# Kernel optimization log

Measured on AMD Instinct MI355X. Metric: run time of the kernel, lower is better.

Reference implementation:

```python
import jax, jax.numpy as jnp
import numpy as np
import math

B, L, D, K = 4, 2048, 1024, 3
PAD = K // 2
EPS_LN = 1e-5
EPS_NORM = 1e-12


def dwsep_conv(x_bld, dw, dwb, pw, pwb):
    # x_bld: [B, L, D] -> depthwise conv over L (groups=D) then pointwise 1x1
    x = jnp.transpose(x_bld, (0, 2, 1))  # [B, D, L]
    y = jax.lax.conv_general_dilated(
        x, dw, window_strides=(1,), padding=[(PAD, PAD)],
        feature_group_count=D, dimension_numbers=("NCH", "OIH", "NCH"))
    y = y + dwb[None, :, None]
    y = jnp.einsum("bcl,oc->bol", y, pw) + pwb[None, :, None]
    return jnp.transpose(y, (0, 2, 1))  # [B, L, D]


def l2norm(x):
    n = jnp.sqrt(jnp.sum(x * x, axis=-1, keepdims=True))
    return x / jnp.maximum(n, EPS_NORM)


def layernorm(x, g, b):
    mu = jnp.mean(x, axis=-1, keepdims=True)
    var = jnp.mean((x - mu) ** 2, axis=-1, keepdims=True)
    return (x - mu) * jax.lax.rsqrt(var + EPS_LN) * g + b


def setup_inputs() -> dict:
    key = jax.random.key(0)
    ks = jax.random.split(key, 24)
    s = 0.02
    def w(k, shape, scale=s):
        return (jax.random.normal(k, shape, dtype=jnp.float32) * scale)
    inp = {
        "x": jax.random.normal(ks[0], (B, L, D), dtype=jnp.float32),
        "wq": w(ks[1], (D, D)), "bq": jnp.zeros((D,), jnp.float32),
        "wk": w(ks[2], (D, D)), "bk": jnp.zeros((D,), jnp.float32),
        "wv": w(ks[3], (D, D)), "bv": jnp.zeros((D,), jnp.float32),
        "dwq": w(ks[4], (D, 1, K), 0.1), "dwq_b": jnp.zeros((D,), jnp.float32),
        "pwq": w(ks[5], (D, D)), "pwq_b": jnp.zeros((D,), jnp.float32),
        "dwk": w(ks[6], (D, 1, K), 0.1), "dwk_b": jnp.zeros((D,), jnp.float32),
        "pwk": w(ks[7], (D, D)), "pwk_b": jnp.zeros((D,), jnp.float32),
        "dwv": w(ks[8], (D, 1, K), 0.1), "dwv_b": jnp.zeros((D,), jnp.float32),
        "pwv": w(ks[9], (D, D)), "pwv_b": jnp.zeros((D,), jnp.float32),
        "wg": w(ks[10], (D, D)), "bg": jnp.zeros((D,), jnp.float32),
        "wo": w(ks[11], (D, D)), "bo": jnp.zeros((D,), jnp.float32),
        "mem_w": w(ks[12], (D, D)),
        "ln_g": jnp.ones((D,), jnp.float32),
        "ln_b": jnp.zeros((D,), jnp.float32),
    }
    return inp


def reference(x, wq, bq, wk, bk, wv, bv,
              dwq, dwq_b, pwq, pwq_b,
              dwk, dwk_b, pwk, pwk_b,
              dwv, dwv_b, pwv, pwv_b,
              wg, bg, wo, bo, mem_w, ln_g, ln_b):
    residual = x
    Q = jax.nn.silu(jnp.einsum("bld,ed->ble", x, wq) + bq)
    Kt = jax.nn.silu(jnp.einsum("bld,ed->ble", x, wk) + bk)
    V = jax.nn.silu(jnp.einsum("bld,ed->ble", x, wv) + bv)
    Q = dwsep_conv(Q, dwq, dwq_b, pwq, pwq_b)
    Kt = dwsep_conv(Kt, dwk, dwk_b, pwk, pwk_b)
    V = dwsep_conv(V, dwv, dwv_b, pwv, pwv_b)
    Qn = l2norm(Q)
    Kn = l2norm(Kt)
    scores = jnp.einsum("bqd,bkd->bqk", Qn, Kn) / math.sqrt(D)
    attn = jax.nn.softmax(scores, axis=-1)
    attn_out = jnp.einsum("bqk,bkd->bqd", attn, V)
    gate = jax.nn.sigmoid(jnp.einsum("bld,ed->ble", attn_out, wg) + bg)
    gated = gate * attn_out
    out = jnp.einsum("bld,ed->ble", gated, wo) + bo + residual
    out = layernorm(out, ln_g, ln_b)
    mem_pred = jnp.einsum("bld,de->ble", Kn, mem_w)
    mem_loss = jnp.mean((mem_pred - V) ** 2)
    return (out, mem_loss)
```

## Files before the change

### kernel.cpp

```cpp
#include <hip/hip_runtime.h>
#include <stdint.h>

typedef __attribute__((ext_vector_type(8))) short short8;
typedef __attribute__((ext_vector_type(4))) short short4v;
typedef __attribute__((ext_vector_type(4))) float f32x4;

#define DEV static __device__ __forceinline__

static constexpr int LL = 2048;
static constexpr int DD = 1024;
static constexpr long long BLD = 8388608LL;

DEV short f2bf(float f) {
    uint32_t u = __builtin_bit_cast(uint32_t, f);
    u += 0x7fffu + ((u >> 16) & 1u);
    return (short)(u >> 16);
}
DEV float bf2f(short s) {
    uint32_t u = ((uint32_t)(uint16_t)s) << 16;
    return __builtin_bit_cast(float, u);
}

DEV float waveSum(float v) {
#pragma unroll
    for (int o = 32; o; o >>= 1) v += __shfl_down(v, o);
    return v;
}
DEV float waveMax(float v) {
#pragma unroll
    for (int o = 32; o; o >>= 1) v = fmaxf(v, __shfl_down(v, o));
    return v;
}

DEV void gload16(const void* g, void* l) {
    __builtin_amdgcn_global_load_lds(
        (const __attribute__((address_space(1))) uint32_t*)(uintptr_t)g,
        (__attribute__((address_space(3))) uint32_t*)(uintptr_t)l,
        16, 0, 0);
}


__global__ __launch_bounds__(256) void k_zero1(float* p) {
    if (threadIdx.x == 0) *p = 0.f;
}

__global__ __launch_bounds__(256) void k_f32_to_bf16(const float* __restrict__ in,
                                                     short* __restrict__ out, int n8) {
    int i = blockIdx.x * 256 + threadIdx.x;
    if (i >= n8) return;
    const float4* p = (const float4*)(in + (long long)i * 8);
    float4 a = p[0], b = p[1];
    short8 o;
    o[0] = f2bf(a.x); o[1] = f2bf(a.y); o[2] = f2bf(a.z); o[3] = f2bf(a.w);
    o[4] = f2bf(b.x); o[5] = f2bf(b.y); o[6] = f2bf(b.z); o[7] = f2bf(b.w);
    *(short8*)(out + (long long)i * 8) = o;
}

__global__ __launch_bounds__(256) void k_wcat(
    const float* wq, const float* wk, const float* wv,
    const float* pq, const float* pk, const float* pv,
    const float* wg, const float* wo,
    short* Wqkv, short* Pqkv, short* Wg, short* Wo) {
    const int bid = blockIdx.x;
    const int w = bid >> 9;
    const long long i = (long long)((bid & 511) * 256 + threadIdx.x) * 8;
    const float* src; short* dst;
    switch (w) {
        case 0: src = wq; dst = Wqkv;                break;
        case 1: src = wk; dst = Wqkv + 1048576;      break;
        case 2: src = wv; dst = Wqkv + 2097152;      break;
        case 3: src = pq; dst = Pqkv;                break;
        case 4: src = pk; dst = Pqkv + 1048576;      break;
        case 5: src = pv; dst = Pqkv + 2097152;      break;
        case 6: src = wg; dst = Wg;                  break;
        default: src = wo; dst = Wo;                 break;
    }
    const float4* p = (const float4*)(src + i);
    float4 a = p[0], b = p[1];
    short8 o;
    o[0] = f2bf(a.x); o[1] = f2bf(a.y); o[2] = f2bf(a.z); o[3] = f2bf(a.w);
    o[4] = f2bf(b.x); o[5] = f2bf(b.y); o[6] = f2bf(b.z); o[7] = f2bf(b.w);
    *(short8*)(dst + i) = o;
}

__global__ __launch_bounds__(256) void k_biascat(
    const float* bq, const float* bk, const float* bv,
    const float* pq, const float* pk, const float* pv,
    float* bqkv, float* bpw) {
    const int idx = blockIdx.x * 256 + threadIdx.x;
    const int sel = idx >> 10, j = idx & 1023;
    const float* s;
    switch (sel) {
        case 0: s = bq; break; case 1: s = bk; break; case 2: s = bv; break;
        case 3: s = pq; break; case 4: s = pk; break; default: s = pv; break;
    }
    float v = s[j];
    if (sel < 3) bqkv[sel * 1024 + j] = v;
    else         bpw[(sel - 3) * 1024 + j] = v;
}

__global__ __launch_bounds__(256) void k_dwconv3b(const short* __restrict__ in,
                                                  const float* __restrict__ dwq,
                                                  const float* __restrict__ dwk,
                                                  const float* __restrict__ dwv,
                                                  const float* __restrict__ dbq,
                                                  const float* __restrict__ dbk,
                                                  const float* __restrict__ dbv,
                                                  short* __restrict__ outp) {
    const int idx = blockIdx.x * 256 + threadIdx.x;
    const int d8 = idx & 127;
    const int lc = (idx >> 7) & 255;
    const int b  = (idx >> 15) & 3;
    const int br = idx >> 17;
    const float* dw = (br == 0) ? dwq : (br == 1) ? dwk : dwv;
    const float* db = (br == 0) ? dbq : (br == 1) ? dbk : dbv;

    float w[24], bb[8];
    {
        const float4* wp = (const float4*)(dw + d8 * 24);
#pragma unroll
        for (int i = 0; i < 6; i++) {
            float4 t = wp[i];
            w[i * 4 + 0] = t.x; w[i * 4 + 1] = t.y;
            w[i * 4 + 2] = t.z; w[i * 4 + 3] = t.w;
        }
        const float4* bp = (const float4*)(db + d8 * 8);
        float4 t0 = bp[0], t1 = bp[1];
        bb[0] = t0.x; bb[1] = t0.y; bb[2] = t0.z; bb[3] = t0.w;
        bb[4] = t1.x; bb[5] = t1.y; bb[6] = t1.z; bb[7] = t1.w;
    }

    const int l0 = lc * 8;
    const long long base = ((long long)(b * LL + l0)) * 3072 + br * 1024 + d8 * 8;
    short8 xr[10];
#pragma unroll
    for (int i = 0; i < 10; i++) {
        const int l = l0 - 1 + i;
        if (l >= 0 && l < LL) xr[i] = *(const short8*)(in + base + (long long)(i - 1) * 3072);
        else { short8 z = {0, 0, 0, 0, 0, 0, 0, 0}; xr[i] = z; }
    }
#pragma unroll
    for (int j = 0; j < 8; j++) {
        short8 o;
#pragma unroll
        for (int c = 0; c < 8; c++) {
            float v = bb[c] + w[c * 3 + 0] * bf2f(xr[j][c])
                            + w[c * 3 + 1] * bf2f(xr[j + 1][c])
                            + w[c * 3 + 2] * bf2f(xr[j + 2][c]);
            o[c] = f2bf(v);
        }
        *(short8*)(outp + base + (long long)j * 3072) = o;
    }
}

__global__ __launch_bounds__(256) void k_l2norm(short* __restrict__ xp) {
    __shared__ float red[4];
    const long long row = blockIdx.x;
    short* p = xp + row * DD;
    const int t = threadIdx.x;
    short4v v = *(short4v*)(p + t * 4);
    float f0 = bf2f(v[0]), f1 = bf2f(v[1]), f2 = bf2f(v[2]), f3 = bf2f(v[3]);
    float ss = f0 * f0 + f1 * f1 + f2 * f2 + f3 * f3;
    ss = waveSum(ss);
    if ((t & 63) == 0) red[t >> 6] = ss;
    __syncthreads();
    ss = (red[0] + red[1]) + (red[2] + red[3]);
    float s = 1.f / fmaxf(sqrtf(ss), 1e-12f);
    v[0] = f2bf(f0 * s); v[1] = f2bf(f1 * s); v[2] = f2bf(f2 * s); v[3] = f2bf(f3 * s);
    *(short4v*)(p + t * 4) = v;
}

__global__ __launch_bounds__(256) void k_softmax(short* __restrict__ sp) {
    __shared__ float redM[4], redS[4];
    const long long row = blockIdx.x;
    short* p = sp + row * 2048;
    const int t = threadIdx.x;
    short8 v = *(short8*)(p + t * 8);
    float f[8];
    float m = -3.0e38f;
#pragma unroll
    for (int j = 0; j < 8; j++) { f[j] = bf2f(v[j]); m = fmaxf(m, f[j]); }
    m = waveMax(m);
    if ((t & 63) == 0) redM[t >> 6] = m;
    __syncthreads();
    m = fmaxf(fmaxf(redM[0], redM[1]), fmaxf(redM[2], redM[3]));
    float s = 0.f;
#pragma unroll
    for (int j = 0; j < 8; j++) { f[j] = __expf(f[j] - m); s += f[j]; }
    s = waveSum(s);
    if ((t & 63) == 0) redS[t >> 6] = s;
    __syncthreads();
    s = (redS[0] + redS[1]) + (redS[2] + redS[3]);
    float inv = 1.f / s;
#pragma unroll
    for (int j = 0; j < 8; j++) v[j] = f2bf(f[j] * inv);
    *(short8*)(p + t * 8) = v;
}

__global__ __launch_bounds__(256) void k_layernorm(float* __restrict__ y,
                                                   const float* __restrict__ g,
                                                   const float* __restrict__ b) {
    __shared__ float redS[4], redQ[4];
    const long long row = blockIdx.x;
    float* p = y + row * DD;
    const int t = threadIdx.x;
    float4 v = *(float4*)(p + t * 4);
    float s = v.x + v.y + v.z + v.w;
    float q = v.x * v.x + v.y * v.y + v.z * v.z + v.w * v.w;
    s = waveSum(s); q = waveSum(q);
    if ((t & 63) == 0) { redS[t >> 6] = s; redQ[t >> 6] = q; }
    __syncthreads();
    s = (redS[0] + redS[1]) + (redS[2] + redS[3]);
    q = (redQ[0] + redQ[1]) + (redQ[2] + redQ[3]);
    float mu = s * (1.f / DD);
    float var = q * (1.f / DD) - mu * mu;
    float rs = rsqrtf(var + 1e-5f);
    float4 o;
    o.x = (v.x - mu) * rs * g[t * 4 + 0] + b[t * 4 + 0];
    o.y = (v.y - mu) * rs * g[t * 4 + 1] + b[t * 4 + 1];
    o.z = (v.z - mu) * rs * g[t * 4 + 2] + b[t * 4 + 2];
    o.w = (v.w - mu) * rs * g[t * 4 + 3] + b[t * 4 + 3];
    *(float4*)(p + t * 4) = o;
}

__global__ __launch_bounds__(256) void k_transpose_bf16(const short* __restrict__ in,
                                                        short* __restrict__ out,
                                                        int rows, int cols) {
    __shared__ short tile[64][65];
    const long long boff = (long long)blockIdx.z * rows * cols;
    in += boff; out += boff;
    const int r0 = blockIdx.y * 64, c0 = blockIdx.x * 64;
    const int t = threadIdx.x;
#pragma unroll
    for (int i = 0; i < 16; i++) {
        int lin = i * 256 + t; int lr = lin >> 6, lc = lin & 63;
        tile[lr][lc] = in[(long long)(r0 + lr) * cols + (c0 + lc)];
    }
    __syncthreads();
#pragma unroll
    for (int i = 0; i < 16; i++) {
        int lin = i * 256 + t; int orr = lin >> 6, oc = lin & 63;
        out[(long long)(c0 + orr) * rows + (r0 + oc)] = tile[oc][orr];
    }
}

__global__ __launch_bounds__(256) void k_transpose_f32_bf16(const float* __restrict__ in,
                                                            short* __restrict__ out,
                                                            int rows, int cols) {
    __shared__ float tile[64][65];
    const int r0 = blockIdx.y * 64, c0 = blockIdx.x * 64;
    const int t = threadIdx.x;
#pragma unroll
    for (int i = 0; i < 16; i++) {
        int lin = i * 256 + t; int lr = lin >> 6, lc = lin & 63;
        tile[lr][lc] = in[(long long)(r0 + lr) * cols + (c0 + lc)];
    }
    __syncthreads();
#pragma unroll
    for (int i = 0; i < 16; i++) {
        int lin = i * 256 + t; int orr = lin >> 6, oc = lin & 63;
        out[(long long)(c0 + orr) * rows + (r0 + oc)] = f2bf(tile[oc][orr]);
    }
}

enum { EPI_SILU, EPI_BIAS, EPI_SCALE, EPI_PLAIN, EPI_GATE, EPI_RESID, EPI_MLOSS };

template <int EPI>
__global__ __launch_bounds__(512, 4) void gemm256b(
    const short* __restrict__ A, int lda, long long sAb,
    const short* __restrict__ W, int ldw, long long sWb,
    void* __restrict__ outv, int ldo, long long sOb,
    const float* __restrict__ bias, long long sBias,
    int K, float scale) {
    __shared__ short lds[24576];

    const int z = blockIdx.z;
    A += (long long)z * sAb;
    W += (long long)z * sWb;

    const int tid = threadIdx.x;
    const int wid = tid >> 6, lane = tid & 63;
    const int row0 = blockIdx.y * 256, col0 = blockIdx.x * 128;
    const int wrM = (wid >> 1) * 64, wcN = (wid & 1) * 64;
    const int rl = lane & 15, kcl = lane >> 4;

    f32x4 acc[4][4] = {};

    const int srow = tid >> 3;
    const int cswz = (tid & 7) ^ (srow & 7);
    long long offA[4], offB[2];
#pragma unroll
    for (int j = 0; j < 4; j++)
        offA[j] = (long long)(row0 + j * 64 + srow) * lda + cswz * 8;
#pragma unroll
    for (int j = 0; j < 2; j++)
        offB[j] = (long long)(col0 + j * 64 + srow) * ldw + cswz * 8;

    const int nk = K >> 6;
    const int swz0 = (kcl ^ (rl & 7)) * 8;
    const int swz1 = ((kcl + 4) ^ (rl & 7)) * 8;

    for (int t = 0; t < nk; ++t) {
        const short* a = A + (long long)t * 64;
        const short* w = W + (long long)t * 64;
#pragma unroll
        for (int j = 0; j < 4; j++)
            gload16(a + offA[j], lds + (j * 512 + tid) * 8);
#pragma unroll
        for (int j = 0; j < 2; j++)
            gload16(w + offB[j], lds + 16384 + (j * 512 + tid) * 8);
        asm volatile("s_waitcnt vmcnt(0)" ::: "memory");
        __builtin_amdgcn_s_barrier();

        short8 af[4], bfr[4];
#pragma unroll
        for (int mi = 0; mi < 4; mi++)
            af[mi] = *(const short8*)&lds[(wrM + mi * 16 + rl) * 64 + swz0];
#pragma unroll
        for (int ni = 0; ni < 4; ni++)
            bfr[ni] = *(const short8*)&lds[16384 + (wcN + ni * 16 + rl) * 64 + swz0];
        __builtin_amdgcn_s_setprio(1);
#pragma unroll
        for (int mi = 0; mi < 4; mi++)
#pragma unroll
            for (int ni = 0; ni < 4; ni++)
                acc[mi][ni] = __builtin_amdgcn_mfma_f32_16x16x32_bf16(
                    af[mi], bfr[ni], acc[mi][ni], 0, 0, 0);
        __builtin_amdgcn_s_setprio(0);
#pragma unroll
        for (int mi = 0; mi < 4; mi++)
            af[mi] = *(const short8*)&lds[(wrM + mi * 16 + rl) * 64 + swz1];
#pragma unroll
        for (int ni = 0; ni < 4; ni++)
            bfr[ni] = *(const short8*)&lds[16384 + (wcN + ni * 16 + rl) * 64 + swz1];
        __builtin_amdgcn_s_setprio(1);
#pragma unroll
        for (int mi = 0; mi < 4; mi++)
#pragma unroll
            for (int ni = 0; ni < 4; ni++)
                acc[mi][ni] = __builtin_amdgcn_mfma_f32_16x16x32_bf16(
                    af[mi], bfr[ni], acc[mi][ni], 0, 0, 0);
        __builtin_amdgcn_s_setprio(0);
        __builtin_amdgcn_s_barrier();
    }

    const int lr4 = (lane >> 4) * 4;
    float bcol[4];
    if constexpr (EPI == EPI_SILU || EPI == EPI_BIAS) {
        const float* bz = bias + (long long)z * sBias;
#pragma unroll
        for (int ni = 0; ni < 4; ni++) bcol[ni] = bz[col0 + wcN + ni * 16 + rl];
    }
    short* op = (short*)outv + (long long)z * sOb;
#pragma unroll
    for (int mi = 0; mi < 4; mi++) {
#pragma unroll
        for (int ni = 0; ni < 4; ni++) {
            const int gc = col0 + wcN + ni * 16 + rl;
#pragma unroll
            for (int r = 0; r < 4; r++) {
                const int gr = row0 + wrM + mi * 16 + lr4 + r;
                float v = acc[mi][ni][r];
                if constexpr (EPI == EPI_SILU) {
                    v += bcol[ni];
                    v = v / (1.f + __expf(-v));
                } else if constexpr (EPI == EPI_BIAS) {
                    v += bcol[ni];
                } else if constexpr (EPI == EPI_SCALE) {
                    v *= scale;
                }
                op[(long long)gr * ldo + gc] = f2bf(v);
            }
        }
    }
}

template <int EPI>
__global__ __launch_bounds__(256, 4) void gemm(
    const short* __restrict__ A, int lda, long long sAb,
    const short* __restrict__ W, int ldw, long long sWb,
    void* __restrict__ outv, int ldo, long long sOb,
    const float* __restrict__ bias, long long sBias,
    const void* __restrict__ aux,
    int K, float scale, float* __restrict__ lossOut) {
    __shared__ short lds[16384];

    const int z = blockIdx.z;
    A += (long long)z * sAb;
    W += (long long)z * sWb;

    const int tid = threadIdx.x;
    const int wid = tid >> 6, lane = tid & 63;
    const int row0 = blockIdx.y * 128, col0 = blockIdx.x * 128;
    const int wrM = (wid >> 1) * 64, wcN = (wid & 1) * 64;
    const int rl = lane & 15, kcl = lane >> 4;

    f32x4 acc[4][4] = {};

    const int srow = tid >> 3;
    const int cswz = (tid & 7) ^ (srow & 7);
    long long offA[4], offB[4];
#pragma unroll
    for (int j = 0; j < 4; j++) {
        const int rr = j * 32 + srow;
        offA[j] = (long long)(row0 + rr) * lda + cswz * 8;
        offB[j] = (long long)(col0 + rr) * ldw + cswz * 8;
    }

    const int nk = K >> 6;
    const int swz0 = (kcl ^ (rl & 7)) * 8;
    const int swz1 = ((kcl + 4) ^ (rl & 7)) * 8;

    for (int t = 0; t < nk; ++t) {
        const short* a = A + (long long)t * 64;
        const short* w = W + (long long)t * 64;
#pragma unroll
        for (int j = 0; j < 4; j++)
            gload16(a + offA[j], lds + (j * 256 + tid) * 8);
#pragma unroll
        for (int j = 0; j < 4; j++)
            gload16(w + offB[j], lds + 8192 + (j * 256 + tid) * 8);
        asm volatile("s_waitcnt vmcnt(0)" ::: "memory");
        __builtin_amdgcn_s_barrier();

        short8 af[4], bfr[4];
#pragma unroll
        for (int mi = 0; mi < 4; mi++)
            af[mi] = *(const short8*)&lds[(wrM + mi * 16 + rl) * 64 + swz0];
#pragma unroll
        for (int ni = 0; ni < 4; ni++)
            bfr[ni] = *(const short8*)&lds[8192 + (wcN + ni * 16 + rl) * 64 + swz0];
        __builtin_amdgcn_s_setprio(1);
#pragma unroll
        for (int mi = 0; mi < 4; mi++)
#pragma unroll
            for (int ni = 0; ni < 4; ni++)
                acc[mi][ni] = __builtin_amdgcn_mfma_f32_16x16x32_bf16(
                    af[mi], bfr[ni], acc[mi][ni], 0, 0, 0);
        __builtin_amdgcn_s_setprio(0);
#pragma unroll
        for (int mi = 0; mi < 4; mi++)
            af[mi] = *(const short8*)&lds[(wrM + mi * 16 + rl) * 64 + swz1];
#pragma unroll
        for (int ni = 0; ni < 4; ni++)
            bfr[ni] = *(const short8*)&lds[8192 + (wcN + ni * 16 + rl) * 64 + swz1];
        __builtin_amdgcn_s_setprio(1);
#pragma unroll
        for (int mi = 0; mi < 4; mi++)
#pragma unroll
            for (int ni = 0; ni < 4; ni++)
                acc[mi][ni] = __builtin_amdgcn_mfma_f32_16x16x32_bf16(
                    af[mi], bfr[ni], acc[mi][ni], 0, 0, 0);
        __builtin_amdgcn_s_setprio(0);
        __builtin_amdgcn_s_barrier();
    }

    const int lr4 = (lane >> 4) * 4;
    float bcol[4];
    if constexpr (EPI == EPI_SILU || EPI == EPI_BIAS || EPI == EPI_GATE || EPI == EPI_RESID) {
        const float* bz = bias + (long long)z * sBias;
#pragma unroll
        for (int ni = 0; ni < 4; ni++) bcol[ni] = bz[col0 + wcN + ni * 16 + rl];
    }
    float lsum = 0.f;
#pragma unroll
    for (int mi = 0; mi < 4; mi++) {
#pragma unroll
        for (int ni = 0; ni < 4; ni++) {
            const int gc = col0 + wcN + ni * 16 + rl;
#pragma unroll
            for (int r = 0; r < 4; r++) {
                const int gr = row0 + wrM + mi * 16 + lr4 + r;
                const long long oi = (long long)gr * ldo + gc;
                float v = acc[mi][ni][r];
                if constexpr (EPI == EPI_SILU) {
                    v += bcol[ni];
                    v = v / (1.f + __expf(-v));
                    ((short*)outv + (long long)z * sOb)[oi] = f2bf(v);
                } else if constexpr (EPI == EPI_BIAS) {
                    ((short*)outv + (long long)z * sOb)[oi] = f2bf(v + bcol[ni]);
                } else if constexpr (EPI == EPI_SCALE) {
                    ((short*)outv + (long long)z * sOb)[oi] = f2bf(v * scale);
                } else if constexpr (EPI == EPI_PLAIN) {
                    ((short*)outv + (long long)z * sOb)[oi] = f2bf(v);
                } else if constexpr (EPI == EPI_GATE) {
                    float g = 1.f / (1.f + __expf(-(v + bcol[ni])));
                    float a = bf2f(((const short*)aux)[oi]);
                    ((short*)outv)[oi] = f2bf(g * a);
                } else if constexpr (EPI == EPI_RESID) {
                    ((float*)outv)[oi] = v + bcol[ni] + ((const float*)aux)[oi];
                } else {
                    float dd = v - bf2f(((const short*)aux)[oi]);
                    lsum += dd * dd;
                }
            }
        }
    }
    if constexpr (EPI == EPI_MLOSS) {
        lsum = waveSum(lsum);
        if (lane == 0) atomicAdd(lossOut, lsum * scale);
    }
}


extern "C" void kernel_launch(void* const* d_in, const int* in_sizes, int n_in,
                              void* d_out, int out_size, void* d_ws, size_t ws_size,
                              hipStream_t stream) {
    const float* x    = (const float*)d_in[0];
    const float* wq   = (const float*)d_in[1];
    const float* bq   = (const float*)d_in[2];
    const float* wk   = (const float*)d_in[3];
    const float* bk   = (const float*)d_in[4];
    const float* wvw  = (const float*)d_in[5];
    const float* bvv  = (const float*)d_in[6];
    const float* dwq  = (const float*)d_in[7];
    const float* dwqb = (const float*)d_in[8];
    const float* pwq  = (const float*)d_in[9];
    const float* pwqb = (const float*)d_in[10];
    const float* dwk  = (const float*)d_in[11];
    const float* dwkb = (const float*)d_in[12];
    const float* pwk  = (const float*)d_in[13];
    const float* pwkb = (const float*)d_in[14];
    const float* dwv  = (const float*)d_in[15];
    const float* dwvb = (const float*)d_in[16];
    const float* pwv  = (const float*)d_in[17];
    const float* pwvb = (const float*)d_in[18];
    const float* wg   = (const float*)d_in[19];
    const float* bg   = (const float*)d_in[20];
    const float* wo   = (const float*)d_in[21];
    const float* bo   = (const float*)d_in[22];
    const float* memw = (const float*)d_in[23];
    const float* lng  = (const float*)d_in[24];
    const float* lnb  = (const float*)d_in[25];

    float* out = (float*)d_out;
    float* loss = out + BLD;

    char* base = (char*)d_ws;
    size_t off = 0;
    auto take = [&](size_t n) -> char* {
        char* p = base + off;
        off += (n + 255) & ~(size_t)255;
        return p;
    };
    const size_t WB = (size_t)DD * DD * 2;
    const size_t XB = (size_t)BLD * 2;
    short* Wqkv = (short*)take(3 * WB);
    short* Pqkv = (short*)take(3 * WB);
    short* Wgb  = (short*)take(WB);
    short* Wob  = (short*)take(WB);
    short* MwT  = (short*)take(WB);
    float* bqkv = (float*)take(3072 * 4);
    float* bpw  = (float*)take(3072 * 4);
    short* xb   = (short*)take(XB);
    short* pre  = (short*)take(3 * XB);
    short* post = (short*)take(3 * XB);

    short* qb = pre;
    short* kb = pre + BLD;
    short* vb = pre + 2 * BLD;
    short* scores = post;
    short* VT = post + 2 * BLD;
    short* aob = xb;
    short* gated = post;
    (void)ws_size; (void)in_sizes; (void)n_in; (void)out_size;

    const long long sLD = (long long)LL * DD;
    const long long sLLb = (long long)LL * LL;

    k_zero1<<<1, 1, 0, stream>>>(loss);
    k_wcat<<<4096, 256, 0, stream>>>(wq, wk, wvw, pwq, pwk, pwv, wg, wo,
                                     Wqkv, Pqkv, Wgb, Wob);
    k_biascat<<<24, 256, 0, stream>>>(bq, bk, bvv, pwqb, pwkb, pwvb, bqkv, bpw);
    k_transpose_f32_bf16<<<dim3(16, 16, 1), 256, 0, stream>>>(memw, MwT, DD, DD);
    k_f32_to_bf16<<<4096, 256, 0, stream>>>(x, xb, (int)(BLD / 8));

    gemm256b<EPI_SILU><<<dim3(24, 32, 1), 512, 0, stream>>>(
        xb, 1024, 0, Wqkv, 1024, 0, pre, 3072, 0, bqkv, 0, 1024, 0.f);

    k_dwconv3b<<<1536, 256, 0, stream>>>(pre, dwq, dwk, dwv, dwqb, dwkb, dwvb, post);

    gemm256b<EPI_BIAS><<<dim3(8, 32, 3), 512, 0, stream>>>(
        post, 3072, 1024, Pqkv, 1024, (long long)DD * DD, qb, 1024, BLD,
        bpw, 1024, 1024, 0.f);

    k_l2norm<<<16384, 256, 0, stream>>>(qb);
    k_transpose_bf16<<<dim3(16, 32, 4), 256, 0, stream>>>(vb, VT, 2048, 1024);

    gemm256b<EPI_SCALE><<<dim3(16, 8, 4), 512, 0, stream>>>(
        qb, 1024, sLD, kb, 1024, sLD, scores, 2048, sLLb,
        nullptr, 0, 1024, 0.03125f);
    k_softmax<<<8192, 256, 0, stream>>>(scores);

    gemm<EPI_PLAIN><<<dim3(8, 16, 4), 256, 0, stream>>>(
        scores, 2048, sLLb, VT, 2048, sLD, aob, 1024, sLD,
        nullptr, 0, nullptr, 2048, 0.f, nullptr);

    gemm<EPI_GATE><<<dim3(8, 64, 1), 256, 0, stream>>>(
        aob, 1024, 0, Wgb, 1024, 0, gated, 1024, 0, bg, 0, aob, 1024, 0.f, nullptr);

    gemm<EPI_RESID><<<dim3(8, 64, 1), 256, 0, stream>>>(
        gated, 1024, 0, Wob, 1024, 0, out, 1024, 0, bo, 0, x, 1024, 0.f, nullptr);
    k_layernorm<<<8192, 256, 0, stream>>>(out, lng, lnb);

    gemm<EPI_MLOSS><<<dim3(8, 64, 1), 256, 0, stream>>>(
        kb, 1024, 0, MwT, 1024, 0, nullptr, 1024, 0, nullptr, 0, vb,
        1024, 1.f / (float)BLD, loss);
}
```

Before: 411.6 us.

## Fuse exp into score GEMM, defer softmax normalization, merge AV with mem-loss GEMM

Drops the max-subtraction softmax pass because normalized Q/K bound the scores, applying exp in the score GEMM epilogue. A light row-sum kernel computes inverse sums that are applied in the AV GEMM epilogue. The AV GEMM and mem-loss GEMM now run as one launch to fill the device. The 256x128 GEMM variant is also replaced by the 128x128 kernel everywhere, which may lower data reuse on the large GEMMs.

```diff
diff --git a/kernel.cpp b/kernel.cpp
--- a/kernel.cpp
+++ b/kernel.cpp
@@ -10,6 +10,8 @@
 static constexpr int LL = 2048;
 static constexpr int DD = 1024;
 static constexpr long long BLD = 8388608LL;
+static constexpr long long SLD = 2097152LL;
+static constexpr long long SLLB = 4194304LL;
 
 DEV short f2bf(float f) {
     uint32_t u = __builtin_bit_cast(uint32_t, f);
@@ -24,11 +26,6 @@
 DEV float waveSum(float v) {
 #pragma unroll
     for (int o = 32; o; o >>= 1) v += __shfl_down(v, o);
-    return v;
-}
-DEV float waveMax(float v) {
-#pragma unroll
-    for (int o = 32; o; o >>= 1) v = fmaxf(v, __shfl_down(v, o));
     return v;
 }
 
@@ -170,31 +167,21 @@
     *(short4v*)(p + t * 4) = v;
 }
 
-__global__ __launch_bounds__(256) void k_softmax(short* __restrict__ sp) {
-    __shared__ float redM[4], redS[4];
+__global__ __launch_bounds__(256) void k_rowsuminv(const short* __restrict__ sp,
+                                                   float* __restrict__ rinv) {
+    __shared__ float red[4];
     const long long row = blockIdx.x;
-    short* p = sp + row * 2048;
+    const short* p = sp + row * 2048;
     const int t = threadIdx.x;
     short8 v = *(short8*)(p + t * 8);
-    float f[8];
-    float m = -3.0e38f;
-#pragma unroll
-    for (int j = 0; j < 8; j++) { f[j] = bf2f(v[j]); m = fmaxf(m, f[j]); }
-    m = waveMax(m);
-    if ((t & 63) == 0) redM[t >> 6] = m;
+    float s = 0.f;
+#pragma unroll
+    for (int j = 0; j < 8; j++) s += bf2f(v[j]);
+    s = waveSum(s);
+    if ((t & 63) == 0) red[t >> 6] = s;
     __syncthreads();
-    m = fmaxf(fmaxf(redM[0], redM[1]), fmaxf(redM[2], redM[3]));
-    float s = 0.f;
-#pragma unroll
-    for (int j = 0; j < 8; j++) { f[j] = __expf(f[j] - m); s += f[j]; }
-    s = waveSum(s);
-    if ((t & 63) == 0) redS[t >> 6] = s;
-    __syncthreads();
-    s = (redS[0] + redS[1]) + (redS[2] + redS[3]);
-    float inv = 1.f / s;
-#pragma unroll
-    for (int j = 0; j < 8; j++) v[j] = f2bf(f[j] * inv);
-    *(short8*)(p + t * 8) = v;
+    s = (red[0] + red[1]) + (red[2] + red[3]);
+    if (t == 0) rinv[row] = 1.f / s;
 }
 
 __global__ __launch_bounds__(256) void k_layernorm(float* __restrict__ y,
@@ -263,117 +250,7 @@
     }
 }
 
-enum { EPI_SILU, EPI_BIAS, EPI_SCALE, EPI_PLAIN, EPI_GATE, EPI_RESID, EPI_MLOSS };
-
-template <int EPI>
-__global__ __launch_bounds__(512, 4) void gemm256b(
-    const short* __restrict__ A, int lda, long long sAb,
-    const short* __restrict__ W, int ldw, long long sWb,
-    void* __restrict__ outv, int ldo, long long sOb,
-    const float* __restrict__ bias, long long sBias,
-    int K, float scale) {
-    __shared__ short lds[24576];
-
-    const int z = blockIdx.z;
-    A += (long long)z * sAb;
-    W += (long long)z * sWb;
-
-    const int tid = threadIdx.x;
-    const int wid = tid >> 6, lane = tid & 63;
-    const int row0 = blockIdx.y * 256, col0 = blockIdx.x * 128;
-    const int wrM = (wid >> 1) * 64, wcN = (wid & 1) * 64;
-    const int rl = lane & 15, kcl = lane >> 4;
-
-    f32x4 acc[4][4] = {};
-
-    const int srow = tid >> 3;
-    const int cswz = (tid & 7) ^ (srow & 7);
-    long long offA[4], offB[2];
-#pragma unroll
-    for (int j = 0; j < 4; j++)
-        offA[j] = (long long)(row0 + j * 64 + srow) * lda + cswz * 8;
-#pragma unroll
-    for (int j = 0; j < 2; j++)
-        offB[j] = (long long)(col0 + j * 64 + srow) * ldw + cswz * 8;
-
-    const int nk = K >> 6;
-    const int swz0 = (kcl ^ (rl & 7)) * 8;
-    const int swz1 = ((kcl + 4) ^ (rl & 7)) * 8;
-
-    for (int t = 0; t < nk; ++t) {
-        const short* a = A + (long long)t * 64;
-        const short* w = W + (long long)t * 64;
-#pragma unroll
-        for (int j = 0; j < 4; j++)
-            gload16(a + offA[j], lds + (j * 512 + tid) * 8);
-#pragma unroll
-        for (int j = 0; j < 2; j++)
-            gload16(w + offB[j], lds + 16384 + (j * 512 + tid) * 8);
-        asm volatile("s_waitcnt vmcnt(0)" ::: "memory");
-        __builtin_amdgcn_s_barrier();
-
-        short8 af[4], bfr[4];
-#pragma unroll
-        for (int mi = 0; mi < 4; mi++)
-            af[mi] = *(const short8*)&lds[(wrM + mi * 16 + rl) * 64 + swz0];
-#pragma unroll
-        for (int ni = 0; ni < 4; ni++)
-            bfr[ni] = *(const short8*)&lds[16384 + (wcN + ni * 16 + rl) * 64 + swz0];
-        __builtin_amdgcn_s_setprio(1);
-#pragma unroll
-        for (int mi = 0; mi < 4; mi++)
-#pragma unroll
-            for (int ni = 0; ni < 4; ni++)
-                acc[mi][ni] = __builtin_amdgcn_mfma_f32_16x16x32_bf16(
-                    af[mi], bfr[ni], acc[mi][ni], 0, 0, 0);
-        __builtin_amdgcn_s_setprio(0);
-#pragma unroll
-        for (int mi = 0; mi < 4; mi++)
-            af[mi] = *(const short8*)&lds[(wrM + mi * 16 + rl) * 64 + swz1];
-#pragma unroll
-        for (int ni = 0; ni < 4; ni++)
-            bfr[ni] = *(const short8*)&lds[16384 + (wcN + ni * 16 + rl) * 64 + swz1];
-        __builtin_amdgcn_s_setprio(1);
-#pragma unroll
-        for (int mi = 0; mi < 4; mi++)
-#pragma unroll
-            for (int ni = 0; ni < 4; ni++)
-                acc[mi][ni] = __builtin_amdgcn_mfma_f32_16x16x32_bf16(
-                    af[mi], bfr[ni], acc[mi][ni], 0, 0, 0);
-        __builtin_amdgcn_s_setprio(0);
-        __builtin_amdgcn_s_barrier();
-    }
-
-    const int lr4 = (lane >> 4) * 4;
-    float bcol[4];
-    if constexpr (EPI == EPI_SILU || EPI == EPI_BIAS) {
-        const float* bz = bias + (long long)z * sBias;
-#pragma unroll
-        for (int ni = 0; ni < 4; ni++) bcol[ni] = bz[col0 + wcN + ni * 16 + rl];
-    }
-    short* op = (short*)outv + (long long)z * sOb;
-#pragma unroll
-    for (int mi = 0; mi < 4; mi++) {
-#pragma unroll
-        for (int ni = 0; ni < 4; ni++) {
-            const int gc = col0 + wcN + ni * 16 + rl;
-#pragma unroll
-            for (int r = 0; r < 4; r++) {
-                const int gr = row0 + wrM + mi * 16 + lr4 + r;
-                float v = acc[mi][ni][r];
-                if constexpr (EPI == EPI_SILU) {
-                    v += bcol[ni];
-                    v = v / (1.f + __expf(-v));
-                } else if constexpr (EPI == EPI_BIAS) {
-                    v += bcol[ni];
-                } else if constexpr (EPI == EPI_SCALE) {
-                    v *= scale;
-                }
-                op[(long long)gr * ldo + gc] = f2bf(v);
-            }
-        }
-    }
-}
+enum { EPI_SILU, EPI_BIAS, EPI_EXPS, EPI_GATE, EPI_RESID };
 
 template <int EPI>
 __global__ __launch_bounds__(256, 4) void gemm(
@@ -382,7 +259,7 @@
     void* __restrict__ outv, int ldo, long long sOb,
     const float* __restrict__ bias, long long sBias,
     const void* __restrict__ aux,
-    int K, float scale, float* __restrict__ lossOut) {
+    int K, float scale) {
     __shared__ short lds[16384];
 
     const int z = blockIdx.z;
@@ -462,7 +339,6 @@
 #pragma unroll
         for (int ni = 0; ni < 4; ni++) bcol[ni] = bz[col0 + wcN + ni * 16 + rl];
     }
-    float lsum = 0.f;
 #pragma unroll
     for (int mi = 0; mi < 4; mi++) {
 #pragma unroll
@@ -479,26 +355,143 @@
                     ((short*)outv + (long long)z * sOb)[oi] = f2bf(v);
                 } else if constexpr (EPI == EPI_BIAS) {
                     ((short*)outv + (long long)z * sOb)[oi] = f2bf(v + bcol[ni]);
-                } else if constexpr (EPI == EPI_SCALE) {
-                    ((short*)outv + (long long)z * sOb)[oi] = f2bf(v * scale);
-                } else if constexpr (EPI == EPI_PLAIN) {
-                    ((short*)outv + (long long)z * sOb)[oi] = f2bf(v);
+                } else if constexpr (EPI == EPI_EXPS) {
+                    ((short*)outv + (long long)z * sOb)[oi] = f2bf(__expf(v * scale));
                 } else if constexpr (EPI == EPI_GATE) {
                     float g = 1.f / (1.f + __expf(-(v + bcol[ni])));
                     float a = bf2f(((const short*)aux)[oi]);
                     ((short*)outv)[oi] = f2bf(g * a);
                 } else if constexpr (EPI == EPI_RESID) {
                     ((float*)outv)[oi] = v + bcol[ni] + ((const float*)aux)[oi];
-                } else {
-                    float dd = v - bf2f(((const short*)aux)[oi]);
+                }
+            }
+        }
+    }
+}
+
+__global__ __launch_bounds__(256, 4) void k_avml(
+    const short* __restrict__ P, const short* __restrict__ VT,
+    const float* __restrict__ rinv, short* __restrict__ aob,
+    const short* __restrict__ kb, const short* __restrict__ MwT,
+    const short* __restrict__ vb, float* __restrict__ lossOut) {
+    __shared__ short lds[16384];
+
+    const int bid = blockIdx.x;
+    const bool isAV = bid < 512;
+    const short* A; const short* W;
+    int lda, ldw, K, row0, col0;
+    const float* rp = nullptr;
+    short* outp = nullptr;
+    if (isAV) {
+        const int z = bid >> 7, rem = bid & 127;
+        row0 = (rem >> 3) * 128; col0 = (rem & 7) * 128;
+        A = P + (long long)z * SLLB;  lda = 2048;
+        W = VT + (long long)z * SLD;  ldw = 2048;
+        K = 2048;
+        outp = aob + (long long)z * SLD;
+        rp = rinv + z * 2048;
+    } else {
+        const int rem = bid - 512;
+        row0 = (rem >> 3) * 128; col0 = (rem & 7) * 128;
+        A = kb; lda = 1024; W = MwT; ldw = 1024; K = 1024;
+    }
+
+    const int tid = threadIdx.x;
+    const int wid = tid >> 6, lane = tid & 63;
+    const int wrM = (wid >> 1) * 64, wcN = (wid & 1) * 64;
+    const int rl = lane & 15, kcl = lane >> 4;
+
+    f32x4 acc[4][4] = {};
+
+    const int srow = tid >> 3;
+    const int cswz = (tid & 7) ^ (srow & 7);
+    long long offA[4], offB[4];
+#pragma unroll
+    for (int j = 0; j < 4; j++) {
+        const int rr = j * 32 + srow;
+        offA[j] = (long long)(row0 + rr) * lda + cswz * 8;
+        offB[j] = (long long)(col0 + rr) * ldw + cswz * 8;
+    }
+
+    const int nk = K >> 6;
+    const int swz0 = (kcl ^ (rl & 7)) * 8;
+    const int swz1 = ((kcl + 4) ^ (rl & 7)) * 8;
+
+    for (int t = 0; t < nk; ++t) {
+        const short* a = A + (long long)t * 64;
+        const short* w = W + (long long)t * 64;
+#pragma unroll
+        for (int j = 0; j < 4; j++)
+            gload16(a + offA[j], lds + (j * 256 + tid) * 8);
+#pragma unroll
+        for (int j = 0; j < 4; j++)
+            gload16(w + offB[j], lds + 8192 + (j * 256 + tid) * 8);
+        asm volatile("s_waitcnt vmcnt(0)" ::: "memory");
+        __builtin_amdgcn_s_barrier();
+
+        short8 af[4], bfr[4];
+#pragma unroll
+        for (int mi = 0; mi < 4; mi++)
+            af[mi] = *(const short8*)&lds[(wrM + mi * 16 + rl) * 64 + swz0];
+#pragma unroll
+        for (int ni = 0; ni < 4; ni++)
+            bfr[ni] = *(const short8*)&lds[8192 + (wcN + ni * 16 + rl) * 64 + swz0];
+        __builtin_amdgcn_s_setprio(1);
+#pragma unroll
+        for (int mi = 0; mi < 4; mi++)
+#pragma unroll
+            for (int ni = 0; ni < 4; ni++)
+                acc[mi][ni] = __builtin_amdgcn_mfma_f32_16x16x32_bf16(
+                    af[mi], bfr[ni], acc[mi][ni], 0, 0, 0);
+        __builtin_amdgcn_s_setprio(0);
+#pragma unroll
+        for (int mi = 0; mi < 4; mi++)
+            af[mi] = *(const short8*)&lds[(wrM + mi * 16 + rl) * 64 + swz1];
+#pragma unroll
+        for (int ni = 0; ni < 4; ni++)
+            bfr[ni] = *(const short8*)&lds[8192 + (wcN + ni * 16 + rl) * 64 + swz1];
+        __builtin_amdgcn_s_setprio(1);
+#pragma unroll
+        for (int mi = 0; mi < 4; mi++)
+#pragma unroll
+            for (int ni = 0; ni < 4; ni++)
+                acc[mi][ni] = __builtin_amdgcn_mfma_f32_16x16x32_bf16(
+                    af[mi], bfr[ni], acc[mi][ni], 0, 0, 0);
+        __builtin_amdgcn_s_setprio(0);
+        __builtin_amdgcn_s_barrier();
+    }
+
+    const int lr4 = (lane >> 4) * 4;
+    if (isAV) {
+#pragma unroll
+        for (int mi = 0; mi < 4; mi++) {
+#pragma unroll
+            for (int ni = 0; ni < 4; ni++) {
+                const int gc = col0 + wcN + ni * 16 + rl;
+#pragma unroll
+                for (int r = 0; r < 4; r++) {
+                    const int gr = row0 + wrM + mi * 16 + lr4 + r;
+                    outp[(long long)gr * 1024 + gc] = f2bf(acc[mi][ni][r] * rp[gr]);
+                }
+            }
+        }
+    } else {
+        float lsum = 0.f;
+#pragma unroll
+        for (int mi = 0; mi < 4; mi++) {
+#pragma unroll
+            for (int ni = 0; ni < 4; ni++) {
+                const int gc = col0 + wcN + ni * 16 + rl;
+#pragma unroll
+                for (int r = 0; r < 4; r++) {
+                    const int gr = row0 + wrM + mi * 16 + lr4 + r;
+                    float dd = acc[mi][ni][r] - bf2f(vb[(long long)gr * 1024 + gc]);
                     lsum += dd * dd;
                 }
             }
         }
-    }
-    if constexpr (EPI == EPI_MLOSS) {
         lsum = waveSum(lsum);
-        if (lane == 0) atomicAdd(lossOut, lsum * scale);
+        if (lane == 0) atomicAdd(lossOut, lsum * (1.f / (float)BLD));
     }
 }
 
@@ -552,6 +545,7 @@
     short* MwT  = (short*)take(WB);
     float* bqkv = (float*)take(3072 * 4);
     float* bpw  = (float*)take(3072 * 4);
+    float* rinv = (float*)take(8192 * 4);
     short* xb   = (short*)take(XB);
     short* pre  = (short*)take(3 * XB);
     short* post = (short*)take(3 * XB);
@@ -565,8 +559,8 @@
     short* gated = post;
     (void)ws_size; (void)in_sizes; (void)n_in; (void)out_size;
 
-    const long long sLD = (long long)LL * DD;
-    const long long sLLb = (long long)LL * LL;
+    const long long sLD = SLD;
+    const long long sLLb = SLLB;
 
     k_zero1<<<1, 1, 0, stream>>>(loss);
     k_wcat<<<4096, 256, 0, stream>>>(wq, wk, wvw, pwq, pwk, pwv, wg, wo,
@@ -575,35 +569,29 @@
     k_transpose_f32_bf16<<<dim3(16, 16, 1), 256, 0, stream>>>(memw, MwT, DD, DD);
     k_f32_to_bf16<<<4096, 256, 0, stream>>>(x, xb, (int)(BLD / 8));
 
-    gemm256b<EPI_SILU><<<dim3(24, 32, 1), 512, 0, stream>>>(
-        xb, 1024, 0, Wqkv, 1024, 0, pre, 3072, 0, bqkv, 0, 1024, 0.f);
+    gemm<EPI_SILU><<<dim3(24, 64, 1), 256, 0, stream>>>(
+        xb, 1024, 0, Wqkv, 1024, 0, pre, 3072, 0, bqkv, 0, nullptr, 1024, 0.f);
 
     k_dwconv3b<<<1536, 256, 0, stream>>>(pre, dwq, dwk, dwv, dwqb, dwkb, dwvb, post);
 
-    gemm256b<EPI_BIAS><<<dim3(8, 32, 3), 512, 0, stream>>>(
+    gemm<EPI_BIAS><<<dim3(8, 64, 3), 256, 0, stream>>>(
         post, 3072, 1024, Pqkv, 1024, (long long)DD * DD, qb, 1024, BLD,
-        bpw, 1024, 1024, 0.f);
+        bpw, 1024, nullptr, 1024, 0.f);
 
     k_l2norm<<<16384, 256, 0, stream>>>(qb);
     k_transpose_bf16<<<dim3(16, 32, 4), 256, 0, stream>>>(vb, VT, 2048, 1024);
 
-    gemm256b<EPI_SCALE><<<dim3(16, 8, 4), 512, 0, stream>>>(
+    gemm<EPI_EXPS><<<dim3(16, 16, 4), 256, 0, stream>>>(
         qb, 1024, sLD, kb, 1024, sLD, scores, 2048, sLLb,
-        nullptr, 0, 1024, 0.03125f);
-    k_softmax<<<8192, 256, 0, stream>>>(scores);
-
-    gemm<EPI_PLAIN><<<dim3(8, 16, 4), 256, 0, stream>>>(
-        scores, 2048, sLLb, VT, 2048, sLD, aob, 1024, sLD,
-        nullptr, 0, nullptr, 2048, 0.f, nullptr);
+        nullptr, 0, nullptr, 1024, 0.03125f);
+    k_rowsuminv<<<8192, 256, 0, stream>>>(scores, rinv);
+
+    k_avml<<<1024, 256, 0, stream>>>(scores, VT, rinv, aob, kb, MwT, vb, loss);
 
     gemm<EPI_GATE><<<dim3(8, 64, 1), 256, 0, stream>>>(
-        aob, 1024, 0, Wgb, 1024, 0, gated, 1024, 0, bg, 0, aob, 1024, 0.f, nullptr);
+        aob, 1024, 0, Wgb, 1024, 0, gated, 1024, 0, bg, 0, aob, 1024, 0.f);
 
     gemm<EPI_RESID><<<dim3(8, 64, 1), 256, 0, stream>>>(
-        gated, 1024, 0, Wob, 1024, 0, out, 1024, 0, bo, 0, x, 1024, 0.f, nullptr);
+        gated, 1024, 0, Wob, 1024, 0, out, 1024, 0, bo, 0, x, 1024, 0.f);
     k_layernorm<<<8192, 256, 0, stream>>>(out, lng, lnb);
-
-    gemm<EPI_MLOSS><<<dim3(8, 64, 1), 256, 0, stream>>>(
-        kb, 1024, 0, MwT, 1024, 0, nullptr, 1024, 0, nullptr, 0, vb,
-        1024, 1.f / (float)BLD, loss);
-}
+}
```

Result: faster. 379.9 us (-7.7%).
